# Performance work log

Hardware: AMD Instinct MI355X
Metric: run time of the kernel (lower is better)

The kernel has to match this reference:

```python
import jax, jax.numpy as jnp
import numpy as np

B, N, M = 8, 4096, 4096


def setup_inputs() -> dict:
    key = jax.random.key(0)
    k1, k2 = jax.random.split(key)
    tar = jax.random.normal(k1, (B, N, 3), dtype=jnp.float32)
    src = jax.random.normal(k2, (B, M, 3), dtype=jnp.float32)
    return {"tar": tar, "src": src}


def reference(tar, src):
    # diff: [b, n, m, 3]; dist: [b, n, m] Euclidean norm
    diff = tar[:, :, None, :] - src[:, None, :, :]
    dist = jnp.sqrt(jnp.sum(diff * diff, axis=-1))
    # complete: for each target point, min over source points, mean over n -> [b]
    complete = jnp.mean(jnp.min(dist, axis=2), axis=1)
    # accuracy: for each source point, min over target points, mean over m -> [b]
    accuracy = jnp.mean(jnp.min(dist, axis=1), axis=1)
    # reduction='mean' over batch axis
    complete = jnp.mean(complete, axis=-1)
    accuracy = jnp.mean(accuracy, axis=-1)
    chamfer = 0.5 * (complete + accuracy)
    return (accuracy, complete, chamfer)
```

## Files before the change

kernel.cpp:

```cpp
#include <hip/hip_runtime.h>
#include <math.h>

#define B_ 8
#define BIGF 3.4e38f


__global__ __launch_bounds__(256) void pack_kernel(
    const float* __restrict__ tar, const float* __restrict__ src,
    float4* __restrict__ packT, float4* __restrict__ packS,
    unsigned int* __restrict__ colmin, int N, int M)
{
    const int i = blockIdx.x * 256 + threadIdx.x;
    const int nT = B_ * N, nS = B_ * M;
    if (i < nT) {
        float x = tar[3 * i], y = tar[3 * i + 1], z = tar[3 * i + 2];
        packT[i] = make_float4(-2.f * x, -2.f * y, -2.f * z,
                               fmaf(x, x, fmaf(y, y, z * z)));
    } else if (i < nT + nS) {
        int j = i - nT;
        float x = src[3 * j], y = src[3 * j + 1], z = src[3 * j + 2];
        packS[j] = make_float4(x, y, z, fmaf(x, x, fmaf(y, y, z * z)));
    }
    if (i < nS) colmin[i] = 0x7F800000u;
}

__global__ __launch_bounds__(256) void fused_kernel(
    const float4* __restrict__ packT, const float4* __restrict__ packS,
    unsigned int* __restrict__ colmin, float* __restrict__ partials_c,
    int N, int M)
{
    const int b = blockIdx.y;
    const int strip = blockIdx.x;
    const int t = threadIdx.x;
    const int wave = t >> 6, lane = t & 63;
    const int tx = lane & 15, tyl = lane >> 4;

    const float4* __restrict__ pT = packT + (size_t)b * N + strip * 64;
    const float4* __restrict__ pS = packS + (size_t)b * M;
    unsigned int* __restrict__ cm_out = colmin + (size_t)b * M;

    float4 a[16];
#pragma unroll
    for (int r = 0; r < 16; ++r) a[r] = pT[tyl * 16 + r];
    float rmin[16];
#pragma unroll
    for (int r = 0; r < 16; ++r) rmin[r] = BIGF;

    const int nch = M >> 6;
    int ch = wave;
    float4 p[4], pn[4];
    if (ch < nch) {
#pragma unroll
        for (int cr = 0; cr < 4; ++cr) p[cr] = pS[ch * 64 + cr * 16 + tx];
    }
    for (; ch < nch; ch += 4) {
        const int chn = ch + 4;
        if (chn < nch) {
#pragma unroll
            for (int cr = 0; cr < 4; ++cr) pn[cr] = pS[chn * 64 + cr * 16 + tx];
        }
#pragma unroll
        for (int cp = 0; cp < 4; cp += 2) {
            const float4 P0 = p[cp], P1 = p[cp + 1];
            float c0 = BIGF, c1 = BIGF;
#pragma unroll
            for (int r = 0; r < 16; r += 2) {
                float d00 = fmaf(a[r].x, P0.x, fmaf(a[r].y, P0.y,
                            fmaf(a[r].z, P0.z, P0.w))) + a[r].w;
                float d01 = fmaf(a[r].x, P1.x, fmaf(a[r].y, P1.y,
                            fmaf(a[r].z, P1.z, P1.w))) + a[r].w;
                float d10 = fmaf(a[r+1].x, P0.x, fmaf(a[r+1].y, P0.y,
                            fmaf(a[r+1].z, P0.z, P0.w))) + a[r+1].w;
                float d11 = fmaf(a[r+1].x, P1.x, fmaf(a[r+1].y, P1.y,
                            fmaf(a[r+1].z, P1.z, P1.w))) + a[r+1].w;
                rmin[r]   = fminf(rmin[r],   fminf(d00, d01));
                rmin[r+1] = fminf(rmin[r+1], fminf(d10, d11));
                c0 = fminf(c0, fminf(d00, d10));
                c1 = fminf(c1, fminf(d01, d11));
            }
            c0 = fminf(c0, __shfl_xor(c0, 16));
            c0 = fminf(c0, __shfl_xor(c0, 32));
            c1 = fminf(c1, __shfl_xor(c1, 16));
            c1 = fminf(c1, __shfl_xor(c1, 32));
            if (tyl == 0) {
                atomicMin(&cm_out[ch * 64 + cp * 16 + tx],
                          __float_as_uint(fmaxf(c0, 0.f)));
                atomicMin(&cm_out[ch * 64 + (cp + 1) * 16 + tx],
                          __float_as_uint(fmaxf(c1, 0.f)));
            }
        }
#pragma unroll
        for (int cr = 0; cr < 4; ++cr) p[cr] = pn[cr];
    }

#pragma unroll
    for (int r = 0; r < 16; ++r) {
        float v = rmin[r];
        v = fminf(v, __shfl_xor(v, 1));
        v = fminf(v, __shfl_xor(v, 2));
        v = fminf(v, __shfl_xor(v, 4));
        v = fminf(v, __shfl_xor(v, 8));
        rmin[r] = v;
    }
    __shared__ float wr[4][64];
    if (tx == 0) {
#pragma unroll
        for (int r = 0; r < 16; ++r) wr[wave][tyl * 16 + r] = rmin[r];
    }
    __syncthreads();
    if (wave == 0) {
        float v = fminf(fminf(wr[0][lane], wr[1][lane]),
                        fminf(wr[2][lane], wr[3][lane]));
        float s = sqrtf(fmaxf(v, 0.f));
#pragma unroll
        for (int off = 32; off > 0; off >>= 1) s += __shfl_down(s, off);
        if (lane == 0) partials_c[b * gridDim.x + strip] = s;
    }
}

__global__ __launch_bounds__(256) void colsum_kernel(
    const unsigned int* __restrict__ colmin, float* __restrict__ partials_a,
    int total)
{
    const int gid = blockIdx.x * 256 + threadIdx.x;
    float s = 0.f;
    if (gid < total) s = sqrtf(fmaxf(__uint_as_float(colmin[gid]), 0.f));
#pragma unroll
    for (int off = 32; off > 0; off >>= 1) s += __shfl_down(s, off);
    __shared__ float rs[4];
    if ((threadIdx.x & 63) == 0) rs[threadIdx.x >> 6] = s;
    __syncthreads();
    if (threadIdx.x == 0)
        partials_a[blockIdx.x] = rs[0] + rs[1] + rs[2] + rs[3];
}

__global__ __launch_bounds__(256) void finalize_kernel(
    const float* __restrict__ partials_c, const float* __restrict__ partials_a,
    float* __restrict__ outp, int nc, int na, int N, int M)
{
    const int t = threadIdx.x;
    float sc = 0.f, sa = 0.f;
    for (int i = t; i < nc; i += 256) sc += partials_c[i];
    for (int i = t; i < na; i += 256) sa += partials_a[i];
#pragma unroll
    for (int off = 32; off > 0; off >>= 1) {
        sc += __shfl_down(sc, off);
        sa += __shfl_down(sa, off);
    }
    __shared__ float rc[4], ra[4];
    const int wid = t >> 6, lid = t & 63;
    if (lid == 0) { rc[wid] = sc; ra[wid] = sa; }
    __syncthreads();
    if (t == 0) {
        float complete = (rc[0] + rc[1] + rc[2] + rc[3]) / (float)(B_ * N);
        float accuracy = (ra[0] + ra[1] + ra[2] + ra[3]) / (float)(B_ * M);
        outp[0] = accuracy;
        outp[1] = complete;
        outp[2] = 0.5f * (accuracy + complete);
    }
}

extern "C" void kernel_launch(void* const* d_in, const int* in_sizes, int n_in,
                              void* d_out, int out_size, void* d_ws, size_t ws_size,
                              hipStream_t stream) {
    const float* tar = (const float*)d_in[0];
    const float* src = (const float*)d_in[1];
    const int N = in_sizes[0] / (B_ * 3);
    const int M = in_sizes[1] / (B_ * 3);

    float4* packT = (float4*)d_ws;
    float4* packS = packT + (size_t)B_ * N;
    unsigned int* colmin = (unsigned int*)(packS + (size_t)B_ * M);
    float* partials_c = (float*)(colmin + (size_t)B_ * M);
    const int nstrips = N / 64;
    const int nc = nstrips * B_;
    const int na = (B_ * M + 255) / 256;
    float* partials_a = partials_c + nc;

    pack_kernel<<<dim3((B_ * (N + M) + 255) / 256), dim3(256), 0, stream>>>(
        tar, src, packT, packS, colmin, N, M);

    fused_kernel<<<dim3(nstrips, B_), dim3(256), 0, stream>>>(
        packT, packS, colmin, partials_c, N, M);

    colsum_kernel<<<dim3(na), dim3(256), 0, stream>>>(colmin, partials_a, B_ * M);

    finalize_kernel<<<dim3(1), dim3(256), 0, stream>>>(
        partials_c, partials_a, (float*)d_out, nc, na, N, M);
}
```

Measured before the change: 91.38 us.

## Split column range across blocks and merge row minima with atomics

```diff
diff --git a/kernel.cpp b/kernel.cpp
--- a/kernel.cpp
+++ b/kernel.cpp
@@ -8,7 +8,7 @@
 __global__ __launch_bounds__(256) void pack_kernel(
     const float* __restrict__ tar, const float* __restrict__ src,
     float4* __restrict__ packT, float4* __restrict__ packS,
-    unsigned int* __restrict__ colmin, int N, int M)
+    unsigned int* __restrict__ minarr, int N, int M)
 {
     const int i = blockIdx.x * 256 + threadIdx.x;
     const int nT = B_ * N, nS = B_ * M;
@@ -21,23 +21,25 @@
         float x = src[3 * j], y = src[3 * j + 1], z = src[3 * j + 2];
         packS[j] = make_float4(x, y, z, fmaf(x, x, fmaf(y, y, z * z)));
     }
-    if (i < nS) colmin[i] = 0x7F800000u;
+    if (i < nT + nS) minarr[i] = 0x7F800000u;
 }
 
-__global__ __launch_bounds__(256) void fused_kernel(
+__global__ __launch_bounds__(256, 3) void fused_kernel(
     const float4* __restrict__ packT, const float4* __restrict__ packS,
-    unsigned int* __restrict__ colmin, float* __restrict__ partials_c,
+    unsigned int* __restrict__ rowmin, unsigned int* __restrict__ colmin,
     int N, int M)
 {
-    const int b = blockIdx.y;
+    const int b = blockIdx.z;
     const int strip = blockIdx.x;
+    const int colbase = blockIdx.y * (M / gridDim.y);
+    const int ncols = M / gridDim.y;
     const int t = threadIdx.x;
     const int wave = t >> 6, lane = t & 63;
     const int tx = lane & 15, tyl = lane >> 4;
 
     const float4* __restrict__ pT = packT + (size_t)b * N + strip * 64;
-    const float4* __restrict__ pS = packS + (size_t)b * M;
-    unsigned int* __restrict__ cm_out = colmin + (size_t)b * M;
+    const float4* __restrict__ pS = packS + (size_t)b * M + colbase;
+    unsigned int* __restrict__ cm_out = colmin + (size_t)b * M + colbase;
 
     float4 a[16];
 #pragma unroll
@@ -46,7 +48,7 @@
 #pragma unroll
     for (int r = 0; r < 16; ++r) rmin[r] = BIGF;
 
-    const int nch = M >> 6;
+    const int nch = ncols >> 6;
     int ch = wave;
     float4 p[4], pn[4];
     if (ch < nch) {
@@ -111,49 +113,54 @@
     if (wave == 0) {
         float v = fminf(fminf(wr[0][lane], wr[1][lane]),
                         fminf(wr[2][lane], wr[3][lane]));
-        float s = sqrtf(fmaxf(v, 0.f));
-#pragma unroll
-        for (int off = 32; off > 0; off >>= 1) s += __shfl_down(s, off);
-        if (lane == 0) partials_c[b * gridDim.x + strip] = s;
+        atomicMin(&rowmin[(size_t)b * N + strip * 64 + lane],
+                  __float_as_uint(fmaxf(v, 0.f)));
     }
 }
 
-__global__ __launch_bounds__(256) void colsum_kernel(
-    const unsigned int* __restrict__ colmin, float* __restrict__ partials_a,
-    int total)
+__global__ __launch_bounds__(256) void reduce1_kernel(
+    const unsigned int* __restrict__ rowmin,
+    const unsigned int* __restrict__ colmin,
+    float* __restrict__ partials, int N, int M)
 {
+    const int nt = B_ * N, ns = B_ * M;
     const int gid = blockIdx.x * 256 + threadIdx.x;
-    float s = 0.f;
-    if (gid < total) s = sqrtf(fmaxf(__uint_as_float(colmin[gid]), 0.f));
+    const int stride = gridDim.x * 256;
+    float s_t = 0.f, s_s = 0.f;
+    for (int i = gid; i < nt; i += stride) s_t += sqrtf(__uint_as_float(rowmin[i]));
+    for (int i = gid; i < ns; i += stride) s_s += sqrtf(__uint_as_float(colmin[i]));
 #pragma unroll
-    for (int off = 32; off > 0; off >>= 1) s += __shfl_down(s, off);
-    __shared__ float rs[4];
-    if ((threadIdx.x & 63) == 0) rs[threadIdx.x >> 6] = s;
+    for (int off = 32; off > 0; off >>= 1) {
+        s_t += __shfl_down(s_t, off);
+        s_s += __shfl_down(s_s, off);
+    }
+    __shared__ float rt[4], rs[4];
+    const int wid = threadIdx.x >> 6, lid = threadIdx.x & 63;
+    if (lid == 0) { rt[wid] = s_t; rs[wid] = s_s; }
     __syncthreads();
-    if (threadIdx.x == 0)
-        partials_a[blockIdx.x] = rs[0] + rs[1] + rs[2] + rs[3];
+    if (threadIdx.x == 0) {
+        partials[blockIdx.x]       = rt[0] + rt[1] + rt[2] + rt[3];
+        partials[128 + blockIdx.x] = rs[0] + rs[1] + rs[2] + rs[3];
+    }
 }
 
-__global__ __launch_bounds__(256) void finalize_kernel(
-    const float* __restrict__ partials_c, const float* __restrict__ partials_a,
-    float* __restrict__ outp, int nc, int na, int N, int M)
+__global__ __launch_bounds__(128) void finalize_kernel(
+    const float* __restrict__ partials, float* __restrict__ outp, int N, int M)
 {
     const int t = threadIdx.x;
-    float sc = 0.f, sa = 0.f;
-    for (int i = t; i < nc; i += 256) sc += partials_c[i];
-    for (int i = t; i < na; i += 256) sa += partials_a[i];
+    float s_t = partials[t];
+    float s_s = partials[128 + t];
 #pragma unroll
     for (int off = 32; off > 0; off >>= 1) {
-        sc += __shfl_down(sc, off);
-        sa += __shfl_down(sa, off);
+        s_t += __shfl_down(s_t, off);
+        s_s += __shfl_down(s_s, off);
     }
-    __shared__ float rc[4], ra[4];
-    const int wid = t >> 6, lid = t & 63;
-    if (lid == 0) { rc[wid] = sc; ra[wid] = sa; }
+    __shared__ float rt[2], rs[2];
+    if ((t & 63) == 0) { rt[t >> 6] = s_t; rs[t >> 6] = s_s; }
     __syncthreads();
     if (t == 0) {
-        float complete = (rc[0] + rc[1] + rc[2] + rc[3]) / (float)(B_ * N);
-        float accuracy = (ra[0] + ra[1] + ra[2] + ra[3]) / (float)(B_ * M);
+        float complete = (rt[0] + rt[1]) / (float)(B_ * N);
+        float accuracy = (rs[0] + rs[1]) / (float)(B_ * M);
         outp[0] = accuracy;
         outp[1] = complete;
         outp[2] = 0.5f * (accuracy + complete);
@@ -170,21 +177,21 @@
 
     float4* packT = (float4*)d_ws;
     float4* packS = packT + (size_t)B_ * N;
-    unsigned int* colmin = (unsigned int*)(packS + (size_t)B_ * M);
-    float* partials_c = (float*)(colmin + (size_t)B_ * M);
-    const int nstrips = N / 64;
-    const int nc = nstrips * B_;
-    const int na = (B_ * M + 255) / 256;
-    float* partials_a = partials_c + nc;
+    unsigned int* rowmin = (unsigned int*)(packS + (size_t)B_ * M);
+    unsigned int* colmin = rowmin + (size_t)B_ * N;
+    float* partials = (float*)(colmin + (size_t)B_ * M);
 
     pack_kernel<<<dim3((B_ * (N + M) + 255) / 256), dim3(256), 0, stream>>>(
-        tar, src, packT, packS, colmin, N, M);
+        tar, src, packT, packS, rowmin, N, M);
 
-    fused_kernel<<<dim3(nstrips, B_), dim3(256), 0, stream>>>(
-        packT, packS, colmin, partials_c, N, M);
+    const int nstrips = N / 64;
+    const int csplit  = 4;
+    fused_kernel<<<dim3(nstrips, csplit, B_), dim3(256), 0, stream>>>(
+        packT, packS, rowmin, colmin, N, M);
 
-    colsum_kernel<<<dim3(na), dim3(256), 0, stream>>>(colmin, partials_a, B_ * M);
+    reduce1_kernel<<<dim3(128), dim3(256), 0, stream>>>(
+        rowmin, colmin, partials, N, M);
 
-    finalize_kernel<<<dim3(1), dim3(256), 0, stream>>>(
-        partials_c, partials_a, (float*)d_out, nc, na, N, M);
+    finalize_kernel<<<dim3(1), dim3(128), 0, stream>>>(
+        partials, (float*)d_out, N, M);
 }
```

After: 104.9 us. +14.8%, slower.
